# Performance work log

Hardware: AMD Instinct MI355X
Metric: run time of the kernel (lower is better)

## Reference

```python
import jax, jax.numpy as jnp
import numpy as np

K = 9  # knn kernel_size
SLOPE = 0.01  # LeakyReLU slope inside EdgeConv MLP (PyGraphBipartite default)


def setup_inputs() -> dict:
    key = jax.random.key(0)
    ks = jax.random.split(key, 5)
    B, C, H, W = 8, 96, 64, 64
    x = jax.random.normal(ks[0], (B, C, H, W), dtype=jnp.float32)
    # EdgeConv MLP: Linear(2C -> C), LeakyReLU(0.01), Linear(C -> C)
    W1 = jax.random.normal(ks[1], (2 * C, C), dtype=jnp.float32) * (1.0 / np.sqrt(2 * C))
    b1 = jax.random.normal(ks[2], (C,), dtype=jnp.float32) * 0.01
    W2 = jax.random.normal(ks[3], (C, C), dtype=jnp.float32) * (1.0 / np.sqrt(C))
    b2 = jax.random.normal(ks[4], (C,), dtype=jnp.float32) * 0.01
    return {"x": x, "W1": W1, "b1": b1, "W2": W2, "b2": b2}


def reference(x, W1, b1, W2, b2):
    B, C, H, W = x.shape
    M = H * W
    # flat_nodes: (B,C,H,W) -> per-image node features (B, M, C)
    xf = jnp.transpose(x, (0, 2, 3, 1)).reshape(B, M, C)

    # k-NN graph per image (batch-restricted), loop=True so self is a neighbor (dist 0)
    sq = jnp.sum(xf * xf, axis=-1)  # (B, M)
    dist = sq[:, :, None] + sq[:, None, :] - 2.0 * jnp.einsum("bmc,bnc->bmn", xf, xf)
    _, idx = jax.lax.top_k(-dist, K)  # (B, M, K) neighbor indices per center node

    # gather neighbor features: (B, M, K, C)
    xj = jax.vmap(lambda f, i: f[i])(xf, idx)
    xi = xf[:, :, None, :]  # center node, broadcast over K

    # EdgeConv message: MLP([x_i ; x_j - x_i]), then mean over neighbors
    feat = jnp.concatenate([jnp.broadcast_to(xi, xj.shape), xj - xi], axis=-1)  # (B,M,K,2C)
    h = feat @ W1 + b1
    h = jnp.where(h >= 0, h, SLOPE * h)  # LeakyReLU(0.01)
    h = h @ W2 + b2  # (B, M, K, C)
    out = jnp.mean(h, axis=2)  # mean aggregation -> (B, M, C)

    # norm='none' (Identity), act='relu'
    out = jax.nn.relu(out)

    # unflat_nodes: (B, M, C) -> (B, C, H, W)
    return jnp.transpose(out.reshape(B, H, W, C), (0, 3, 1, 2))
```

## Files before the change

### kernel.cpp

```cpp
#include <hip/hip_runtime.h>

#define B_ 8
#define C_ 96
#define CP_ 104
#define M_ 4096
#define K_ 9

typedef _Float16 f16x8 __attribute__((ext_vector_type(8)));
typedef float f32x4 __attribute__((ext_vector_type(4)));

typedef const __attribute__((address_space(1))) unsigned int* as1_u32p;
typedef __attribute__((address_space(3))) unsigned int* as3_u32p;

__device__ inline void g2lds16(const void* g, void* l) {
  __builtin_amdgcn_global_load_lds((as1_u32p)g, (as3_u32p)l, 16, 0, 0);
}

#define INSERT(dv, nv) do {                                                   \
    const int pz_ = tpos;                                                     \
    _Pragma("unroll")                                                         \
    for (int k_ = 0; k_ < K_; ++k_) if (k_ == pz_) { tv[k_] = (dv); ti[k_] = (nv); } \
    float mx_ = tv[0]; int mp_ = 0;                                           \
    _Pragma("unroll")                                                         \
    for (int k_ = 1; k_ < K_; ++k_) if (tv[k_] > mx_) { mx_ = tv[k_]; mp_ = k_; } \
    tmax = mx_; tpos = mp_;                                                   \
  } while (0)

__global__ __launch_bounds__(256) void prep1_kernel(
    const float* __restrict__ x, float* __restrict__ sq,
    unsigned short* __restrict__ xhi, unsigned short* __restrict__ xlo) {
  __shared__ float Xt[C_][64];
  const int b = blockIdx.y, m0 = blockIdx.x * 64, tid = threadIdx.x;
  const float* xb = x + (size_t)b * C_ * M_;
  for (int i = tid; i < C_ * 16; i += 256) {
    int c = i >> 4, j4 = (i & 15) << 2;
    *(float4*)&Xt[c][j4] = *(const float4*)&xb[(size_t)c * M_ + m0 + j4];
  }
  __syncthreads();
  if (tid < 64) {
    float s = 0.f;
#pragma unroll
    for (int c = 0; c < C_; ++c) { float v = Xt[c][tid]; s += v * v; }
    sq[b * M_ + m0 + tid] = s;
  }
  const int p = tid & 63, part = tid >> 6;
  union { unsigned short u[24]; uint4 q[3]; } hb, lb;
#pragma unroll
  for (int i = 0; i < 24; ++i) {
    float v = Xt[part * 24 + i][p];
    _Float16 h = (_Float16)v;
    _Float16 l = (_Float16)(v - (float)h);
    hb.u[i] = __builtin_bit_cast(unsigned short, h);
    lb.u[i] = __builtin_bit_cast(unsigned short, l);
  }
  size_t base = ((size_t)b * M_ + m0 + p) * CP_ + part * 24;
#pragma unroll
  for (int i = 0; i < 3; ++i) {
    *(uint4*)&xhi[base + i * 8] = hb.q[i];
    *(uint4*)&xlo[base + i * 8] = lb.q[i];
  }
}

__global__ __launch_bounds__(256, 2) void knn_kernel(
    const unsigned short* __restrict__ xhi, const unsigned short* __restrict__ xlo,
    const float* __restrict__ sq, int* __restrict__ idxw) {
  __shared__ struct { unsigned short bhi[64 * CP_]; unsigned short blo[64 * CP_]; } S[2];
  __shared__ float Dt[64 * 65];
  __shared__ float sqc[2][64];
  const int b = blockIdx.y, r0 = blockIdx.x * 64, tid = threadIdx.x;
  const int lane = tid & 63, w = tid >> 6;
  const int fp = lane & 15, kg = lane >> 4;
  const size_t bm = (size_t)b * M_;

  f16x8 ahi[4][3], alo[4][3];
#pragma unroll
  for (int rs = 0; rs < 4; ++rs)
#pragma unroll
    for (int kt = 0; kt < 3; ++kt) {
      size_t off = (bm + r0 + rs * 16 + fp) * CP_ + kt * 32 + kg * 8;
      ahi[rs][kt] = *(const f16x8*)&xhi[off];
      alo[rs][kt] = *(const f16x8*)&xlo[off];
    }

  float tv[K_]; int ti[K_]; float tmax = 3.4e38f; int tpos = 0;
#pragma unroll
  for (int k = 0; k < K_; ++k) { tv[k] = 3.4e38f; ti[k] = 0; }

  auto stage = [&](int n0, int pp) {
    const unsigned short* sh = xhi + (bm + n0) * CP_;
    const unsigned short* sl = xlo + (bm + n0) * CP_;
    unsigned short* dh = S[pp].bhi;
    unsigned short* dl = S[pp].blo;
#pragma unroll
    for (int it = 0; it < 3; ++it) {
      int ch = tid + it * 256;
      g2lds16(sh + ch * 8, dh + ch * 8);
      g2lds16(sl + ch * 8, dl + ch * 8);
    }
    if (tid < 64) {
      int ch = 768 + tid;
      g2lds16(sh + ch * 8, dh + ch * 8);
      g2lds16(sl + ch * 8, dl + ch * 8);
      sqc[pp][tid] = sq[bm + n0 + tid];
    }
  };

  stage(0, 0);
  for (int t = 0; t < 64; ++t) {
    const int n0 = t * 64;
    const int cur = t & 1;
    __syncthreads();

    f16x8 bhi[3], blo[3];
#pragma unroll
    for (int kt = 0; kt < 3; ++kt) {
      int boff = (w * 16 + fp) * CP_ + kt * 32 + kg * 8;
      bhi[kt] = *(const f16x8*)&S[cur].bhi[boff];
      blo[kt] = *(const f16x8*)&S[cur].blo[boff];
    }
    if (t < 63) stage(n0 + 64, cur ^ 1);

    const int colg = w * 16 + fp;
    const float scol = sqc[cur][colg];
#pragma unroll
    for (int rs = 0; rs < 4; ++rs) {
      f32x4 acc = {0.f, 0.f, 0.f, 0.f};
#pragma unroll
      for (int kt = 0; kt < 3; ++kt) {
        acc = __builtin_amdgcn_mfma_f32_16x16x32_f16(ahi[rs][kt], bhi[kt], acc, 0, 0, 0);
        acc = __builtin_amdgcn_mfma_f32_16x16x32_f16(ahi[rs][kt], blo[kt], acc, 0, 0, 0);
        acc = __builtin_amdgcn_mfma_f32_16x16x32_f16(alo[rs][kt], bhi[kt], acc, 0, 0, 0);
      }
#pragma unroll
      for (int r = 0; r < 4; ++r) {
        int row = rs * 16 + kg * 4 + r;
        Dt[row * 65 + colg] = scol - 2.f * acc[r];
      }
    }
    __syncthreads();

    const float* drow = &Dt[lane * 65 + w * 16];
    float b0d = 0.f, b1d = 0.f; int b0n = 0, b1n = 0, bcnt = 0;
#pragma unroll
    for (int j = 0; j < 16; ++j) {
      float d = drow[j];
      if (d < tmax) {
        const int n = n0 + w * 16 + j;
        if (bcnt == 2) {
          if (b0d < tmax) INSERT(b0d, b0n);
          b0d = b1d; b0n = b1n;
          b1d = d;   b1n = n;
        } else if (bcnt == 1) {
          b1d = d; b1n = n; bcnt = 2;
        } else {
          b0d = d; b0n = n; bcnt = 1;
        }
      }
    }
    if (bcnt >= 1 && b0d < tmax) INSERT(b0d, b0n);
    if (bcnt == 2 && b1d < tmax) INSERT(b1d, b1n);
  }

  __syncthreads();
  float* mv = (float*)&S[0];
  int*   mi = (int*)((char*)&S[0] + 64 * 37 * 4);
#pragma unroll
  for (int k = 0; k < K_; ++k) {
    mv[lane * 37 + w * K_ + k] = tv[k];
    mi[lane * 37 + w * K_ + k] = ti[k];
  }
  __syncthreads();
  if (tid < 64) {
    float fv[K_]; int fi[K_];
    float mx = 3.4e38f; int mp = 0;
#pragma unroll
    for (int k = 0; k < K_; ++k) { fv[k] = 3.4e38f; fi[k] = 0; }
    for (int s = 0; s < 36; ++s) {
      float v = mv[tid * 37 + s]; int id = mi[tid * 37 + s];
      if (v < mx) {
#pragma unroll
        for (int k = 0; k < K_; ++k) if (k == mp) { fv[k] = v; fi[k] = id; }
        float m2 = fv[0]; int p2 = 0;
#pragma unroll
        for (int k = 1; k < K_; ++k) if (fv[k] > m2) { m2 = fv[k]; p2 = k; }
        mx = m2; mp = p2;
      }
    }
#pragma unroll
    for (int k = 0; k < K_; ++k)
      idxw[((size_t)b * M_ + r0 + tid) * K_ + k] = fi[k];
  }
}

__global__ __launch_bounds__(256) void prep2_kernel(
    const float* __restrict__ x, const float* __restrict__ W1,
    const float* __restrict__ b1, float* __restrict__ P, float* __restrict__ Q) {
  __shared__ float Xt[C_][64];
  __shared__ float Wt[C_][64];
  const int b = blockIdx.y, m0 = blockIdx.x * 64;
  const int tid = threadIdx.x;
  const float* xb = x + (size_t)b * C_ * M_;

  for (int i = tid; i < C_ * 16; i += 256) {
    int c = i >> 4, j4 = (i & 15) << 2;
    *(float4*)&Xt[c][j4] = *(const float4*)&xb[(size_t)c * M_ + m0 + j4];
  }

  const int ty = tid >> 4, tx = tid & 15;
  for (int t = 0; t < 3; ++t) {
    const int u0 = t * 64;
    __syncthreads();
    for (int i = tid; i < C_ * 64; i += 256) {
      int cin = i >> 6, j = i & 63;
      int u = u0 + j;
      float wv;
      if (u < C_) wv = W1[cin * C_ + u] - W1[(C_ + cin) * C_ + u];
      else        wv = W1[(C_ + cin) * C_ + (u - C_)];
      Wt[cin][j] = wv;
    }
    __syncthreads();
    float acc[4][4] = {};
#pragma unroll 8
    for (int c = 0; c < C_; ++c) {
      float4 rr = *(const float4*)&Xt[c][ty << 2];
      float4 ww = *(const float4*)&Wt[c][tx << 2];
      acc[0][0] += rr.x * ww.x; acc[0][1] += rr.x * ww.y; acc[0][2] += rr.x * ww.z; acc[0][3] += rr.x * ww.w;
      acc[1][0] += rr.y * ww.x; acc[1][1] += rr.y * ww.y; acc[1][2] += rr.y * ww.z; acc[1][3] += rr.y * ww.w;
      acc[2][0] += rr.z * ww.x; acc[2][1] += rr.z * ww.y; acc[2][2] += rr.z * ww.z; acc[2][3] += rr.z * ww.w;
      acc[3][0] += rr.w * ww.x; acc[3][1] += rr.w * ww.y; acc[3][2] += rr.w * ww.z; acc[3][3] += rr.w * ww.w;
    }
#pragma unroll
    for (int i = 0; i < 4; ++i) {
      int m = m0 + (ty << 2) + i;
      size_t base = ((size_t)b * M_ + m) * C_;
#pragma unroll
      for (int j = 0; j < 4; ++j) {
        int u = u0 + (tx << 2) + j;
        float v = acc[i][j];
        if (u < C_) P[base + u] = v + b1[u];
        else        Q[base + (u - C_)] = v;
      }
    }
  }
}

__global__ __launch_bounds__(256) void edge_mlp_kernel(
    const float* __restrict__ P, const float* __restrict__ Q,
    const int* __restrict__ idxw, const float* __restrict__ W2,
    const float* __restrict__ b2, float* __restrict__ out) {
  __shared__ float g_l[C_][64];
  __shared__ float W2t[C_ * C_];
  const int b = blockIdx.y, m0 = blockIdx.x * 64;
  const int tid = threadIdx.x;

  for (int i = tid; i < (C_ * C_) / 4; i += 256)
    *(float4*)&W2t[i * 4] = *(const float4*)&W2[i * 4];

  const int ml = tid & 63, cg = tid >> 6;
  const int m = m0 + ml;
  const float* prow = P + ((size_t)b * M_ + m) * C_ + cg * 24;
  float pr[24];
#pragma unroll
  for (int t = 0; t < 24; t += 4) {
    float4 v = *(const float4*)(prow + t);
    pr[t] = v.x; pr[t + 1] = v.y; pr[t + 2] = v.z; pr[t + 3] = v.w;
  }
  float gacc[24] = {};
  const int* irow = idxw + ((size_t)b * M_ + m) * K_;
#pragma unroll
  for (int k = 0; k < K_; ++k) {
    int j = irow[k];
    const float* qrow = Q + ((size_t)b * M_ + j) * C_ + cg * 24;
#pragma unroll
    for (int t = 0; t < 24; t += 4) {
      float4 qv = *(const float4*)(qrow + t);
      float h;
      h = pr[t + 0] + qv.x; gacc[t + 0] += (h >= 0.f) ? h : 0.01f * h;
      h = pr[t + 1] + qv.y; gacc[t + 1] += (h >= 0.f) ? h : 0.01f * h;
      h = pr[t + 2] + qv.z; gacc[t + 2] += (h >= 0.f) ? h : 0.01f * h;
      h = pr[t + 3] + qv.w; gacc[t + 3] += (h >= 0.f) ? h : 0.01f * h;
    }
  }
#pragma unroll
  for (int t = 0; t < 24; ++t) g_l[cg * 24 + t][ml] = gacc[t] * (1.f / 9.f);
  __syncthreads();

  const int ty = tid >> 4, tx = tid & 15;
  float acc2[4][6] = {};
#pragma unroll 4
  for (int c = 0; c < C_; ++c) {
    float4 rr = *(const float4*)&g_l[c][ty << 2];
    float2 wa = *(const float2*)&W2t[c * C_ + tx * 6];
    float2 wb = *(const float2*)&W2t[c * C_ + tx * 6 + 2];
    float2 wc = *(const float2*)&W2t[c * C_ + tx * 6 + 4];
    float rv[4] = {rr.x, rr.y, rr.z, rr.w};
    float wv[6] = {wa.x, wa.y, wb.x, wb.y, wc.x, wc.y};
#pragma unroll
    for (int i = 0; i < 4; ++i)
#pragma unroll
      for (int j = 0; j < 6; ++j) acc2[i][j] += rv[i] * wv[j];
  }
#pragma unroll
  for (int i = 0; i < 4; ++i) {
    int mm = m0 + (ty << 2) + i;
#pragma unroll
    for (int j = 0; j < 6; ++j) {
      int u = tx * 6 + j;
      float v = acc2[i][j] + b2[u];
      v = fmaxf(v, 0.f);
      out[((size_t)b * C_ + u) * M_ + mm] = v;
    }
  }
}

extern "C" void kernel_launch(void* const* d_in, const int* in_sizes, int n_in,
                              void* d_out, int out_size, void* d_ws, size_t ws_size,
                              hipStream_t stream) {
  const float* x  = (const float*)d_in[0];
  const float* W1 = (const float*)d_in[1];
  const float* b1 = (const float*)d_in[2];
  const float* W2 = (const float*)d_in[3];
  const float* b2 = (const float*)d_in[4];
  float* out = (float*)d_out;

  char* ws = (char*)d_ws;
  float* sq  = (float*)ws;
  int* idxw  = (int*)(ws + 131072);
  unsigned short* xhi = (unsigned short*)(ws + 1310720);
  unsigned short* xlo = (unsigned short*)(ws + 8126464);
  float* P = (float*)(ws + 1310720);
  float* Q = (float*)(ws + 13893632);

  dim3 grid(M_ / 64, B_), blk(256);
  prep1_kernel<<<grid, blk, 0, stream>>>(x, sq, xhi, xlo);
  knn_kernel<<<grid, blk, 0, stream>>>(xhi, xlo, sq, idxw);
  prep2_kernel<<<grid, blk, 0, stream>>>(x, W1, b1, P, Q);
  edge_mlp_kernel<<<grid, blk, 0, stream>>>(P, Q, idxw, W2, b2, out);
}
```

Measured before the change: 294.4 us.

## Swap MFMA operands so distances land in registers, dropping LDS distance tile

Each wave now owns 16 query rows held in registers and loops over candidate tiles from LDS as the other MFMA operand. The accumulator then holds, per lane, distances for that lane's query, so top-k insertion runs directly on the MFMA output. This removes the Dt shared-memory tile, its stores and reads, and one barrier per iteration, and raises launch bounds to 3 blocks per CU. In exchange each lane scans only 16 of 64 candidates per tile, giving more lanes partial top-k lists, and the final merge is remapped to the new query/lane mapping.

```diff
diff --git a/kernel.cpp b/kernel.cpp
--- a/kernel.cpp
+++ b/kernel.cpp
@@ -61,26 +61,23 @@
   }
 }
 
-__global__ __launch_bounds__(256, 2) void knn_kernel(
+__global__ __launch_bounds__(256, 3) void knn_kernel(
     const unsigned short* __restrict__ xhi, const unsigned short* __restrict__ xlo,
     const float* __restrict__ sq, int* __restrict__ idxw) {
   __shared__ struct { unsigned short bhi[64 * CP_]; unsigned short blo[64 * CP_]; } S[2];
-  __shared__ float Dt[64 * 65];
   __shared__ float sqc[2][64];
   const int b = blockIdx.y, r0 = blockIdx.x * 64, tid = threadIdx.x;
   const int lane = tid & 63, w = tid >> 6;
   const int fp = lane & 15, kg = lane >> 4;
   const size_t bm = (size_t)b * M_;
 
-  f16x8 ahi[4][3], alo[4][3];
-#pragma unroll
-  for (int rs = 0; rs < 4; ++rs)
-#pragma unroll
-    for (int kt = 0; kt < 3; ++kt) {
-      size_t off = (bm + r0 + rs * 16 + fp) * CP_ + kt * 32 + kg * 8;
-      ahi[rs][kt] = *(const f16x8*)&xhi[off];
-      alo[rs][kt] = *(const f16x8*)&xlo[off];
-    }
+  f16x8 qhi[3], qlo[3];
+#pragma unroll
+  for (int kt = 0; kt < 3; ++kt) {
+    size_t off = (bm + r0 + w * 16 + fp) * CP_ + kt * 32 + kg * 8;
+    qhi[kt] = *(const f16x8*)&xhi[off];
+    qlo[kt] = *(const f16x8*)&xlo[off];
+  }
 
   float tv[K_]; int ti[K_]; float tmax = 3.4e38f; int tpos = 0;
 #pragma unroll
@@ -110,50 +107,41 @@
     const int n0 = t * 64;
     const int cur = t & 1;
     __syncthreads();
-
-    f16x8 bhi[3], blo[3];
-#pragma unroll
-    for (int kt = 0; kt < 3; ++kt) {
-      int boff = (w * 16 + fp) * CP_ + kt * 32 + kg * 8;
-      bhi[kt] = *(const f16x8*)&S[cur].bhi[boff];
-      blo[kt] = *(const f16x8*)&S[cur].blo[boff];
-    }
     if (t < 63) stage(n0 + 64, cur ^ 1);
 
-    const int colg = w * 16 + fp;
-    const float scol = sqc[cur][colg];
+    float b0d = 0.f, b1d = 0.f; int b0n = 0, b1n = 0, bcnt = 0;
+
 #pragma unroll
     for (int rs = 0; rs < 4; ++rs) {
+      f16x8 nh[3], nl[3];
+#pragma unroll
+      for (int kt = 0; kt < 3; ++kt) {
+        int boff = (rs * 16 + fp) * CP_ + kt * 32 + kg * 8;
+        nh[kt] = *(const f16x8*)&S[cur].bhi[boff];
+        nl[kt] = *(const f16x8*)&S[cur].blo[boff];
+      }
       f32x4 acc = {0.f, 0.f, 0.f, 0.f};
 #pragma unroll
       for (int kt = 0; kt < 3; ++kt) {
-        acc = __builtin_amdgcn_mfma_f32_16x16x32_f16(ahi[rs][kt], bhi[kt], acc, 0, 0, 0);
-        acc = __builtin_amdgcn_mfma_f32_16x16x32_f16(ahi[rs][kt], blo[kt], acc, 0, 0, 0);
-        acc = __builtin_amdgcn_mfma_f32_16x16x32_f16(alo[rs][kt], bhi[kt], acc, 0, 0, 0);
+        acc = __builtin_amdgcn_mfma_f32_16x16x32_f16(nh[kt], qhi[kt], acc, 0, 0, 0);
+        acc = __builtin_amdgcn_mfma_f32_16x16x32_f16(nh[kt], qlo[kt], acc, 0, 0, 0);
+        acc = __builtin_amdgcn_mfma_f32_16x16x32_f16(nl[kt], qhi[kt], acc, 0, 0, 0);
       }
 #pragma unroll
       for (int r = 0; r < 4; ++r) {
-        int row = rs * 16 + kg * 4 + r;
-        Dt[row * 65 + colg] = scol - 2.f * acc[r];
-      }
-    }
-    __syncthreads();
-
-    const float* drow = &Dt[lane * 65 + w * 16];
-    float b0d = 0.f, b1d = 0.f; int b0n = 0, b1n = 0, bcnt = 0;
-#pragma unroll
-    for (int j = 0; j < 16; ++j) {
-      float d = drow[j];
-      if (d < tmax) {
-        const int n = n0 + w * 16 + j;
-        if (bcnt == 2) {
-          if (b0d < tmax) INSERT(b0d, b0n);
-          b0d = b1d; b0n = b1n;
-          b1d = d;   b1n = n;
-        } else if (bcnt == 1) {
-          b1d = d; b1n = n; bcnt = 2;
-        } else {
-          b0d = d; b0n = n; bcnt = 1;
+        const int nrow = rs * 16 + kg * 4 + r;
+        const float d = sqc[cur][nrow] - 2.f * acc[r];
+        if (d < tmax) {
+          const int n = n0 + nrow;
+          if (bcnt == 2) {
+            if (b0d < tmax) INSERT(b0d, b0n);
+            b0d = b1d; b0n = b1n;
+            b1d = d;   b1n = n;
+          } else if (bcnt == 1) {
+            b1d = d; b1n = n; bcnt = 2;
+          } else {
+            b0d = d; b0n = n; bcnt = 1;
+          }
         }
       }
     }
@@ -164,10 +152,11 @@
   __syncthreads();
   float* mv = (float*)&S[0];
   int*   mi = (int*)((char*)&S[0] + 64 * 37 * 4);
+  const int qrow = w * 16 + fp;
 #pragma unroll
   for (int k = 0; k < K_; ++k) {
-    mv[lane * 37 + w * K_ + k] = tv[k];
-    mi[lane * 37 + w * K_ + k] = ti[k];
+    mv[qrow * 37 + kg * K_ + k] = tv[k];
+    mi[qrow * 37 + kg * K_ + k] = ti[k];
   }
   __syncthreads();
   if (tid < 64) {
```

Result: no change. 297.2 us (+0.9%).
